# Optimization experiments

Measured on AMD Instinct MI355X. Metric: run time of the kernel, lower is better.

Reference implementation:

```python
import jax, jax.numpy as jnp
import numpy as np

N_NODES = 20000
N_EDGES = 640000
F = 64       # n_features
B = 20       # n_basis
LN_EPS = 1e-5

act = jax.nn.silu

def _lin_init(key, fan_in, fan_out):
    return jax.random.normal(key, (fan_in, fan_out), dtype=jnp.float32) / np.sqrt(fan_in)

def setup_inputs() -> dict:
    key = jax.random.key(0)
    ks = jax.random.split(key, 18)
    inp = {
        "atom_node": jax.random.normal(ks[0], (N_NODES, F), dtype=jnp.float32),
        "force_node": jax.random.normal(ks[1], (N_NODES, 3, F), dtype=jnp.float32),
        "dir_edge": jax.random.normal(ks[2], (N_EDGES, 3), dtype=jnp.float32),
        "dist_edge": jax.random.uniform(ks[3], (N_EDGES, B), dtype=jnp.float32),
        "edge_index": jax.random.randint(ks[4], (2, N_EDGES), 0, N_NODES, dtype=jnp.int64),
        # message_nodepart: Linear(F,F)+act+Linear(F,F)
        "W1": _lin_init(ks[5], F, F), "b1": jnp.zeros((F,), jnp.float32),
        "W2": _lin_init(ks[6], F, F), "b2": jnp.zeros((F,), jnp.float32),
        # message_edgepart: Linear(B,F,bias=False)
        "We": _lin_init(ks[7], B, F),
        # equiv_message1/2: Linear(F,F,nobias)+act+Linear(F,F,nobias)
        "Wq1a": _lin_init(ks[8], F, F), "Wq1b": _lin_init(ks[9], F, F),
        "Wq2a": _lin_init(ks[10], F, F), "Wq2b": _lin_init(ks[11], F, F),
        # equiv_update: Linear(F,F,nobias)
        "Wu": _lin_init(ks[12], F, F),
        # LayerNorm(F)
        "gamma": jnp.ones((F,), jnp.float32), "beta": jnp.zeros((F,), jnp.float32),
    }
    return inp

def reference(atom_node, force_node, dir_edge, dist_edge, edge_index,
              W1, b1, W2, b2, We, Wq1a, Wq1b, Wq2a, Wq2b, Wu, gamma, beta):
    src, dst = edge_index[0], edge_index[1]
    n = atom_node.shape[0]

    # node part of the message: MLP over nodes [N,F]
    mn = act(atom_node @ W1 + b1) @ W2 + b2
    # edge part: [E,F]
    me = dist_edge @ We
    # message: elementwise product of edge part and both endpoint node parts [E,F]
    message = me * mn[src] * mn[dst]

    # invariant update: scatter-add messages to source nodes
    inv_update1 = jax.ops.segment_sum(message, src, num_segments=n)
    atom_node = atom_node + inv_update1

    # equivariant messages [E,3,F]
    em1_inv = act(message @ Wq1a) @ Wq1b            # [E,F]
    em2_inv = act(message @ Wq2a) @ Wq2b            # [E,F]
    equiv_msg = (em1_inv[:, None, :] * dir_edge[:, :, None]
                 + em2_inv[:, None, :] * force_node[dst])  # [E,3,F]
    force_update = jax.ops.segment_sum(equiv_msg, src, num_segments=n)
    force_node = force_node + force_update

    # invariant contraction of vector features: sum over the 3-dim
    inv_update2 = jnp.sum(force_node * (force_node @ Wu), axis=1)  # [N,F]
    atom_node = atom_node + inv_update2

    # LayerNorm over feature dim
    mu = jnp.mean(atom_node, axis=-1, keepdims=True)
    var = jnp.var(atom_node, axis=-1, keepdims=True)
    atom_node = (atom_node - mu) * jax.lax.rsqrt(var + LN_EPS) * gamma + beta

    return (atom_node, force_node)
```

## Files before the change

### kernel.cpp

```cpp
#include <hip/hip_runtime.h>

#define N_NODES 20000
#define N_EDGES 640000
#define FDIM 64
#define NB 20
#define LN_EPS 1e-5f

typedef __attribute__((ext_vector_type(8))) short bf16x8;
typedef __attribute__((ext_vector_type(4))) float f32x4;

#define SEL_HI 0x07060302u
#define SEL_LO 0x05040100u
#define MFMA16 __builtin_amdgcn_mfma_f32_16x16x32_bf16

__device__ __forceinline__ float silu_f(float x) { return x / (1.0f + __expf(-x)); }

__device__ __forceinline__ float bcast_lane(float v, int lane) {
    return __int_as_float(__builtin_amdgcn_readlane(__float_as_int(v), lane));
}

__device__ __forceinline__ unsigned bf16_rn(float x) {
    unsigned u = __float_as_uint(x);
    return (u + 0x7FFFu + ((u >> 16) & 1u)) >> 16;
}

__device__ __forceinline__ unsigned pack_split(float x) {
    unsigned h = bf16_rn(x);
    unsigned lo = bf16_rn(x - __uint_as_float(h << 16));
    return (h << 16) | lo;
}

__device__ __forceinline__ void load_afrag(const unsigned* rowPtr, int kh, int q,
                                           bf16x8* ahi, bf16x8* alo) {
    const uint4 ra = *(const uint4*)(rowPtr + kh * 32 + q * 8);
    const uint4 rb = *(const uint4*)(rowPtr + kh * 32 + q * 8 + 4);
    union { unsigned u[4]; bf16x8 v; } H, L;
    H.u[0] = __builtin_amdgcn_perm(ra.y, ra.x, SEL_HI);
    H.u[1] = __builtin_amdgcn_perm(ra.w, ra.z, SEL_HI);
    H.u[2] = __builtin_amdgcn_perm(rb.y, rb.x, SEL_HI);
    H.u[3] = __builtin_amdgcn_perm(rb.w, rb.z, SEL_HI);
    L.u[0] = __builtin_amdgcn_perm(ra.y, ra.x, SEL_LO);
    L.u[1] = __builtin_amdgcn_perm(ra.w, ra.z, SEL_LO);
    L.u[2] = __builtin_amdgcn_perm(rb.y, rb.x, SEL_LO);
    L.u[3] = __builtin_amdgcn_perm(rb.w, rb.z, SEL_LO);
    *ahi = H.v;
    *alo = L.v;
}

__device__ __forceinline__ void mm3(const unsigned* Bhi, const unsigned* Blo,
                                    bf16x8 ahi, bf16x8 alo, f32x4* acc, int kh, int l) {
#pragma unroll
    for (int c = 0; c < 4; ++c) {
        bf16x8 bh = *(const bf16x8*)(Bhi + (kh * 4 + c) * 256 + l * 4);
        bf16x8 bl = *(const bf16x8*)(Blo + (kh * 4 + c) * 256 + l * 4);
        acc[c] = MFMA16(ahi, bh, acc[c], 0, 0, 0);
        acc[c] = MFMA16(ahi, bl, acc[c], 0, 0, 0);
        acc[c] = MFMA16(alo, bh, acc[c], 0, 0, 0);
    }
}

__global__ __launch_bounds__(256) void node_mlp_kernel(
    const float* __restrict__ atom, const float* __restrict__ W1, const float* __restrict__ b1,
    const float* __restrict__ W2, const float* __restrict__ b2, float* __restrict__ mn)
{
    __shared__ float W1s[FDIM][FDIM];
    __shared__ float W2s[FDIM][FDIM];
    const int f = threadIdx.x, ty = threadIdx.y;
    const int tid = ty * 64 + f;
    for (int i = tid; i < FDIM * FDIM; i += 256) {
        ((float*)W1s)[i] = W1[i];
        ((float*)W2s)[i] = W2[i];
    }
    __syncthreads();
    const float bb1 = b1[f], bb2 = b2[f];
    const int nw = gridDim.x * 4;
    for (int n = blockIdx.x * 4 + ty; n < N_NODES; n += nw) {
        const float a = atom[n * FDIM + f];
        float h = bb1;
        for (int g = 0; g < FDIM; ++g) h += bcast_lane(a, g) * W1s[g][f];
        h = silu_f(h);
        float o = bb2;
        for (int g = 0; g < FDIM; ++g) o += bcast_lane(h, g) * W2s[g][f];
        mn[n * FDIM + f] = o;
    }
}

__global__ __launch_bounds__(1024, 1) void edge_kernel(
    const float* __restrict__ dist,
    const float* __restrict__ dir,
    const int* __restrict__ eidx,
    const float* __restrict__ mn,
    const float* __restrict__ We,
    const float* __restrict__ Wq1a, const float* __restrict__ Wq1b,
    const float* __restrict__ Wq2a, const float* __restrict__ Wq2b,
    const float* __restrict__ forceN,
    float* __restrict__ atomAcc,
    float* __restrict__ forceAcc)
{
    __shared__ __align__(16) unsigned Bfr[16384];
    __shared__ __align__(16) unsigned WeFr[2048];
    __shared__ __align__(16) unsigned Astg[16][16][76];

    const int l = threadIdx.x;
    const int ty = threadIdx.y;
    const int q = l >> 4, row = l & 15;

    for (int t = ty; t < 32; t += 16) {
        const int mm = t >> 3, kh = (t >> 2) & 1, c = t & 3;
        const float* W = (mm == 0) ? Wq1a : (mm == 1) ? Wq2a : (mm == 2) ? Wq1b : Wq2b;
        const int n = c * 16 + row;
        const int kb = kh * 32 + q * 8;
        unsigned* hiP = &Bfr[(((mm * 2 + 0) * 2 + kh) * 4 + c) * 256 + l * 4];
        unsigned* loP = &Bfr[(((mm * 2 + 1) * 2 + kh) * 4 + c) * 256 + l * 4];
#pragma unroll
        for (int i = 0; i < 4; ++i) {
            float w0 = W[(kb + 2 * i) * FDIM + n];
            float w1 = W[(kb + 2 * i + 1) * FDIM + n];
            unsigned h0 = bf16_rn(w0);
            unsigned l0 = bf16_rn(w0 - __uint_as_float(h0 << 16));
            unsigned h1 = bf16_rn(w1);
            unsigned l1 = bf16_rn(w1 - __uint_as_float(h1 << 16));
            hiP[i] = h0 | (h1 << 16);
            loP[i] = l0 | (l1 << 16);
        }
    }
    for (int c = ty; c < 4; c += 16) {
        const int n = c * 16 + row;
        unsigned* hiP = &WeFr[(0 * 4 + c) * 256 + l * 4];
        unsigned* loP = &WeFr[(1 * 4 + c) * 256 + l * 4];
#pragma unroll
        for (int i = 0; i < 4; ++i) {
            const int k0 = q * 8 + 2 * i, k1 = k0 + 1;
            float w0 = (k0 < NB) ? We[k0 * FDIM + n] : 0.0f;
            float w1 = (k1 < NB) ? We[k1 * FDIM + n] : 0.0f;
            unsigned h0 = bf16_rn(w0);
            unsigned l0 = bf16_rn(w0 - __uint_as_float(h0 << 16));
            unsigned h1 = bf16_rn(w1);
            unsigned l1 = bf16_rn(w1 - __uint_as_float(h1 << 16));
            hiP[i] = h0 | (h1 << 16);
            loP[i] = l0 | (l1 << 16);
        }
    }
    __syncthreads();

    const unsigned* B1aH = Bfr + 0 * 2048; const unsigned* B1aL = Bfr + 1 * 2048;
    const unsigned* B2aH = Bfr + 2 * 2048; const unsigned* B2aL = Bfr + 3 * 2048;
    const unsigned* B1bH = Bfr + 4 * 2048; const unsigned* B1bL = Bfr + 5 * 2048;
    const unsigned* B2bH = Bfr + 6 * 2048; const unsigned* B2bL = Bfr + 7 * 2048;
    const unsigned* WeH = WeFr;            const unsigned* WeL = WeFr + 1024;

    unsigned* stg = &Astg[ty][0][0];
    const unsigned* rowPtr = &Astg[ty][row][0];

    const int ngroups = N_EDGES / 16;
    const int stride = gridDim.x * 16;
    int grp = blockIdx.x * 16 + ty;

    int e0 = grp * 16;
    int evA = (l < 32) ? eidx[(l < 16) ? (e0 + l) : (N_EDGES + e0 + (l - 16))] : 0;
    float dvA = (l < 48) ? dir[e0 * 3 + l] : 0.0f;
    float4 daA = {0.f, 0.f, 0.f, 0.f}, dbA = {0.f, 0.f, 0.f, 0.f};
    {
        const float* dp = dist + (size_t)(e0 + row) * NB + q * 8;
        if (q < 2)       { daA = *(const float4*)dp; dbA = *(const float4*)(dp + 4); }
        else if (q == 2) { daA = *(const float4*)dp; }
    }
    float mnS[16], mnD[16];
#pragma unroll
    for (int j = 0; j < 16; ++j) {
        const int src = __builtin_amdgcn_readlane(evA, j);
        const int dst = __builtin_amdgcn_readlane(evA, 16 + j);
        mnS[j] = mn[(size_t)src * FDIM + l];
        mnD[j] = mn[(size_t)dst * FDIM + l];
    }

    while (grp < ngroups) {
        e0 = grp * 16;
        const int grpN = grp + stride;
        const int e0n = (grpN < ngroups) ? grpN * 16 : 0;

        const int evB = (l < 32) ? eidx[(l < 16) ? (e0n + l) : (N_EDGES + e0n + (l - 16))] : 0;
        const float dvB = (l < 48) ? dir[e0n * 3 + l] : 0.0f;

        unsigned s0 = pack_split(daA.x), s1 = pack_split(daA.y);
        unsigned s2 = pack_split(daA.z), s3 = pack_split(daA.w);
        unsigned s4 = pack_split(dbA.x), s5 = pack_split(dbA.y);
        unsigned s6 = pack_split(dbA.z), s7 = pack_split(dbA.w);
        union { unsigned u[4]; bf16x8 v; } AH, AL;
        AH.u[0] = __builtin_amdgcn_perm(s1, s0, SEL_HI);
        AH.u[1] = __builtin_amdgcn_perm(s3, s2, SEL_HI);
        AH.u[2] = __builtin_amdgcn_perm(s5, s4, SEL_HI);
        AH.u[3] = __builtin_amdgcn_perm(s7, s6, SEL_HI);
        AL.u[0] = __builtin_amdgcn_perm(s1, s0, SEL_LO);
        AL.u[1] = __builtin_amdgcn_perm(s3, s2, SEL_LO);
        AL.u[2] = __builtin_amdgcn_perm(s5, s4, SEL_LO);
        AL.u[3] = __builtin_amdgcn_perm(s7, s6, SEL_LO);

        f32x4 me4[4];
#pragma unroll
        for (int c = 0; c < 4; ++c) me4[c] = (f32x4){0.f, 0.f, 0.f, 0.f};
        mm3(WeH, WeL, AH.v, AL.v, me4, 0, l);
#pragma unroll
        for (int c = 0; c < 4; ++c)
#pragma unroll
            for (int r = 0; r < 4; ++r)
                stg[(q * 4 + r) * 76 + (row + 16 * c)] = __float_as_uint(me4[c][r]);

        float4 daB = {0.f, 0.f, 0.f, 0.f}, dbB = {0.f, 0.f, 0.f, 0.f};
        {
            const float* dpn = dist + (size_t)(e0n + row) * NB + q * 8;
            if (q < 2)       { daB = *(const float4*)dpn; dbB = *(const float4*)(dpn + 4); }
            else if (q == 2) { daB = *(const float4*)dpn; }
        }

#pragma unroll
        for (int j = 0; j < 16; ++j) {
            const int src = __builtin_amdgcn_readlane(evA, j);
            const float me = __uint_as_float(stg[j * 76 + l]);
            const float m = me * mnS[j] * mnD[j];
            atomicAdd(&atomAcc[(size_t)src * FDIM + l], m);
            stg[j * 76 + l] = pack_split(m);
        }

#pragma unroll
        for (int j = 0; j < 16; ++j) {
            const int srcN = __builtin_amdgcn_readlane(evB, j);
            const int dstN = __builtin_amdgcn_readlane(evB, 16 + j);
            mnS[j] = mn[(size_t)srcN * FDIM + l];
            mnD[j] = mn[(size_t)dstN * FDIM + l];
        }

        f32x4 acc1[4], acc2[4];
#pragma unroll
        for (int c = 0; c < 4; ++c) {
            acc1[c] = (f32x4){0.f, 0.f, 0.f, 0.f};
            acc2[c] = (f32x4){0.f, 0.f, 0.f, 0.f};
        }
#pragma unroll
        for (int kh = 0; kh < 2; ++kh) {
            bf16x8 ahi, alo;
            load_afrag(rowPtr, kh, q, &ahi, &alo);
            mm3(B1aH, B1aL, ahi, alo, acc1, kh, l);
            mm3(B2aH, B2aL, ahi, alo, acc2, kh, l);
        }
#pragma unroll
        for (int c = 0; c < 4; ++c)
#pragma unroll
            for (int r = 0; r < 4; ++r) {
                acc1[c][r] = silu_f(acc1[c][r]);
                acc2[c][r] = silu_f(acc2[c][r]);
            }

#pragma unroll
        for (int c = 0; c < 4; ++c)
#pragma unroll
            for (int r = 0; r < 4; ++r)
                stg[(q * 4 + r) * 76 + (row + 16 * c)] = pack_split(acc1[c][r]);
        f32x4 eacc1[4];
#pragma unroll
        for (int c = 0; c < 4; ++c) eacc1[c] = (f32x4){0.f, 0.f, 0.f, 0.f};
#pragma unroll
        for (int kh = 0; kh < 2; ++kh) {
            bf16x8 ahi, alo;
            load_afrag(rowPtr, kh, q, &ahi, &alo);
            mm3(B1bH, B1bL, ahi, alo, eacc1, kh, l);
        }

#pragma unroll
        for (int c = 0; c < 4; ++c)
#pragma unroll
            for (int r = 0; r < 4; ++r)
                stg[(q * 4 + r) * 76 + (row + 16 * c)] = pack_split(acc2[c][r]);
        f32x4 eacc2[4];
#pragma unroll
        for (int c = 0; c < 4; ++c) eacc2[c] = (f32x4){0.f, 0.f, 0.f, 0.f};
#pragma unroll
        for (int kh = 0; kh < 2; ++kh) {
            bf16x8 ahi, alo;
            load_afrag(rowPtr, kh, q, &ahi, &alo);
            mm3(B2bH, B2bL, ahi, alo, eacc2, kh, l);
        }

#pragma unroll
        for (int r = 0; r < 4; ++r) {
            const int eo = q * 4 + r;
            const int vs = __shfl(evA, eo);
            const int vd = __shfl(evA, 16 + eo);
            const float d0 = __shfl(dvA, eo * 3 + 0);
            const float d1 = __shfl(dvA, eo * 3 + 1);
            const float d2 = __shfl(dvA, eo * 3 + 2);
            const float* fd = forceN + (size_t)vd * 3 * FDIM;
            float* fa = forceAcc + (size_t)vs * 3 * FDIM;
#pragma unroll
            for (int c = 0; c < 4; ++c) {
                const int n = row + 16 * c;
                const float a = eacc1[c][r];
                const float b = eacc2[c][r];
                atomicAdd(&fa[0 * FDIM + n], a * d0 + b * fd[0 * FDIM + n]);
                atomicAdd(&fa[1 * FDIM + n], a * d1 + b * fd[1 * FDIM + n]);
                atomicAdd(&fa[2 * FDIM + n], a * d2 + b * fd[2 * FDIM + n]);
            }
        }

        evA = evB;
        dvA = dvB;
        daA = daB;
        dbA = dbB;
        grp = grpN;
    }
}

__global__ __launch_bounds__(256) void node_final_kernel(
    const float* __restrict__ Wu, const float* __restrict__ gamma, const float* __restrict__ beta,
    float* __restrict__ atomAcc, const float* __restrict__ forceOut)
{
    __shared__ float Wus[FDIM][FDIM];
    const int f = threadIdx.x, ty = threadIdx.y;
    const int tid = ty * 64 + f;
    for (int i = tid; i < FDIM * FDIM; i += 256) ((float*)Wus)[i] = Wu[i];
    __syncthreads();
    const float gg = gamma[f], bb = beta[f];
    const int nw = gridDim.x * 4;
    for (int n = blockIdx.x * 4 + ty; n < N_NODES; n += nw) {
        const float f0 = forceOut[((size_t)n * 3 + 0) * FDIM + f];
        const float f1 = forceOut[((size_t)n * 3 + 1) * FDIM + f];
        const float f2 = forceOut[((size_t)n * 3 + 2) * FDIM + f];
        float r0 = 0.0f, r1 = 0.0f, r2 = 0.0f;
#pragma unroll 8
        for (int g = 0; g < FDIM; ++g) {
            const float w = Wus[g][f];
            r0 += bcast_lane(f0, g) * w;
            r1 += bcast_lane(f1, g) * w;
            r2 += bcast_lane(f2, g) * w;
        }
        float a = atomAcc[n * FDIM + f] + (f0 * r0 + f1 * r1 + f2 * r2);
        float s = a;
#pragma unroll
        for (int off = 32; off >= 1; off >>= 1) s += __shfl_xor(s, off, 64);
        const float mu = s * (1.0f / 64.0f);
        const float d = a - mu;
        float v = d * d;
#pragma unroll
        for (int off = 32; off >= 1; off >>= 1) v += __shfl_xor(v, off, 64);
        v *= (1.0f / 64.0f);
        atomAcc[n * FDIM + f] = d * rsqrtf(v + LN_EPS) * gg + bb;
    }
}

extern "C" void kernel_launch(void* const* d_in, const int* in_sizes, int n_in,
                              void* d_out, int out_size, void* d_ws, size_t ws_size,
                              hipStream_t stream)
{
    const float* atom_node  = (const float*)d_in[0];
    const float* force_node = (const float*)d_in[1];
    const float* dir_edge   = (const float*)d_in[2];
    const float* dist_edge  = (const float*)d_in[3];
    const int*   edge_index = (const int*)d_in[4];
    const float* W1   = (const float*)d_in[5];
    const float* b1   = (const float*)d_in[6];
    const float* W2   = (const float*)d_in[7];
    const float* b2   = (const float*)d_in[8];
    const float* We   = (const float*)d_in[9];
    const float* Wq1a = (const float*)d_in[10];
    const float* Wq1b = (const float*)d_in[11];
    const float* Wq2a = (const float*)d_in[12];
    const float* Wq2b = (const float*)d_in[13];
    const float* Wu   = (const float*)d_in[14];
    const float* gamma = (const float*)d_in[15];
    const float* beta  = (const float*)d_in[16];

    float* atomOut  = (float*)d_out;
    float* forceOut = (float*)d_out + (size_t)N_NODES * FDIM;
    float* mn = (float*)d_ws;

    hipMemcpyAsync(atomOut, atom_node, (size_t)N_NODES * FDIM * sizeof(float),
                   hipMemcpyDeviceToDevice, stream);
    hipMemcpyAsync(forceOut, force_node, (size_t)N_NODES * 3 * FDIM * sizeof(float),
                   hipMemcpyDeviceToDevice, stream);

    dim3 blk4(64, 4);
    dim3 blk16(64, 16);
    node_mlp_kernel<<<512, blk4, 0, stream>>>(atom_node, W1, b1, W2, b2, mn);
    edge_kernel<<<256, blk16, 0, stream>>>(dist_edge, dir_edge, edge_index, mn, We,
                                           Wq1a, Wq1b, Wq2a, Wq2b, force_node,
                                           atomOut, forceOut);
    node_final_kernel<<<512, blk4, 0, stream>>>(Wu, gamma, beta, atomOut, forceOut);
}
```

Before: 595.5 us.

## Shrink edge blocks to 8 waves, premultiply node parts, batch force gathers before atomics

Edge blocks go from 16 waves to 8, with launch bounds allowing two blocks per CU. The grid stays at 256 blocks, so total concurrent waves drop by half unless occupancy rises. The src and dst node-part values are multiplied at prefetch time, so one register array replaces two, freeing registers. The next dist prefetch moves earlier in the loop, and the force_node gather loads are grouped ahead of the atomic adds to expose more memory parallelism. The risk is less latency hiding from fewer resident waves, since the grid is not enlarged.

```diff
diff --git a/kernel.cpp b/kernel.cpp
--- a/kernel.cpp
+++ b/kernel.cpp
@@ -5,6 +5,7 @@
 #define FDIM 64
 #define NB 20
 #define LN_EPS 1e-5f
+#define NW 8
 
 typedef __attribute__((ext_vector_type(8))) short bf16x8;
 typedef __attribute__((ext_vector_type(4))) float f32x4;
@@ -85,7 +86,7 @@
     }
 }
 
-__global__ __launch_bounds__(1024, 1) void edge_kernel(
+__global__ __launch_bounds__(64 * NW, 2) void edge_kernel(
     const float* __restrict__ dist,
     const float* __restrict__ dir,
     const int* __restrict__ eidx,
@@ -99,13 +100,13 @@
 {
     __shared__ __align__(16) unsigned Bfr[16384];
     __shared__ __align__(16) unsigned WeFr[2048];
-    __shared__ __align__(16) unsigned Astg[16][16][76];
+    __shared__ __align__(16) unsigned Astg[NW][16][76];
 
     const int l = threadIdx.x;
     const int ty = threadIdx.y;
     const int q = l >> 4, row = l & 15;
 
-    for (int t = ty; t < 32; t += 16) {
+    for (int t = ty; t < 32; t += NW) {
         const int mm = t >> 3, kh = (t >> 2) & 1, c = t & 3;
         const float* W = (mm == 0) ? Wq1a : (mm == 1) ? Wq2a : (mm == 2) ? Wq1b : Wq2b;
         const int n = c * 16 + row;
@@ -124,7 +125,7 @@
             loP[i] = l0 | (l1 << 16);
         }
     }
-    for (int c = ty; c < 4; c += 16) {
+    for (int c = ty; c < 4; c += NW) {
         const int n = c * 16 + row;
         unsigned* hiP = &WeFr[(0 * 4 + c) * 256 + l * 4];
         unsigned* loP = &WeFr[(1 * 4 + c) * 256 + l * 4];
@@ -153,8 +154,8 @@
     const unsigned* rowPtr = &Astg[ty][row][0];
 
     const int ngroups = N_EDGES / 16;
-    const int stride = gridDim.x * 16;
-    int grp = blockIdx.x * 16 + ty;
+    const int stride = gridDim.x * NW;
+    int grp = blockIdx.x * NW + ty;
 
     int e0 = grp * 16;
     int evA = (l < 32) ? eidx[(l < 16) ? (e0 + l) : (N_EDGES + e0 + (l - 16))] : 0;
@@ -165,13 +166,12 @@
         if (q < 2)       { daA = *(const float4*)dp; dbA = *(const float4*)(dp + 4); }
         else if (q == 2) { daA = *(const float4*)dp; }
     }
-    float mnS[16], mnD[16];
+    float pA[16];
 #pragma unroll
     for (int j = 0; j < 16; ++j) {
         const int src = __builtin_amdgcn_readlane(evA, j);
         const int dst = __builtin_amdgcn_readlane(evA, 16 + j);
-        mnS[j] = mn[(size_t)src * FDIM + l];
-        mnD[j] = mn[(size_t)dst * FDIM + l];
+        pA[j] = mn[(size_t)src * FDIM + l] * mn[(size_t)dst * FDIM + l];
     }
 
     while (grp < ngroups) {
@@ -181,6 +181,12 @@
 
         const int evB = (l < 32) ? eidx[(l < 16) ? (e0n + l) : (N_EDGES + e0n + (l - 16))] : 0;
         const float dvB = (l < 48) ? dir[e0n * 3 + l] : 0.0f;
+        float4 daB = {0.f, 0.f, 0.f, 0.f}, dbB = {0.f, 0.f, 0.f, 0.f};
+        {
+            const float* dpn = dist + (size_t)(e0n + row) * NB + q * 8;
+            if (q < 2)       { daB = *(const float4*)dpn; dbB = *(const float4*)(dpn + 4); }
+            else if (q == 2) { daB = *(const float4*)dpn; }
+        }
 
         unsigned s0 = pack_split(daA.x), s1 = pack_split(daA.y);
         unsigned s2 = pack_split(daA.z), s3 = pack_split(daA.w);
@@ -206,18 +212,10 @@
             for (int r = 0; r < 4; ++r)
                 stg[(q * 4 + r) * 76 + (row + 16 * c)] = __float_as_uint(me4[c][r]);
 
-        float4 daB = {0.f, 0.f, 0.f, 0.f}, dbB = {0.f, 0.f, 0.f, 0.f};
-        {
-            const float* dpn = dist + (size_t)(e0n + row) * NB + q * 8;
-            if (q < 2)       { daB = *(const float4*)dpn; dbB = *(const float4*)(dpn + 4); }
-            else if (q == 2) { daB = *(const float4*)dpn; }
-        }
-
 #pragma unroll
         for (int j = 0; j < 16; ++j) {
             const int src = __builtin_amdgcn_readlane(evA, j);
-            const float me = __uint_as_float(stg[j * 76 + l]);
-            const float m = me * mnS[j] * mnD[j];
+            const float m = __uint_as_float(stg[j * 76 + l]) * pA[j];
             atomicAdd(&atomAcc[(size_t)src * FDIM + l], m);
             stg[j * 76 + l] = pack_split(m);
         }
@@ -226,8 +224,7 @@
         for (int j = 0; j < 16; ++j) {
             const int srcN = __builtin_amdgcn_readlane(evB, j);
             const int dstN = __builtin_amdgcn_readlane(evB, 16 + j);
-            mnS[j] = mn[(size_t)srcN * FDIM + l];
-            mnD[j] = mn[(size_t)dstN * FDIM + l];
+            pA[j] = mn[(size_t)srcN * FDIM + l] * mn[(size_t)dstN * FDIM + l];
         }
 
         f32x4 acc1[4], acc2[4];
@@ -290,15 +287,21 @@
             const float d1 = __shfl(dvA, eo * 3 + 1);
             const float d2 = __shfl(dvA, eo * 3 + 2);
             const float* fd = forceN + (size_t)vd * 3 * FDIM;
-            float* fa = forceAcc + (size_t)vs * 3 * FDIM;
+            float f0[4], f1[4], f2[4];
 #pragma unroll
             for (int c = 0; c < 4; ++c) {
                 const int n = row + 16 * c;
-                const float a = eacc1[c][r];
-                const float b = eacc2[c][r];
-                atomicAdd(&fa[0 * FDIM + n], a * d0 + b * fd[0 * FDIM + n]);
-                atomicAdd(&fa[1 * FDIM + n], a * d1 + b * fd[1 * FDIM + n]);
-                atomicAdd(&fa[2 * FDIM + n], a * d2 + b * fd[2 * FDIM + n]);
+                f0[c] = fd[0 * FDIM + n];
+                f1[c] = fd[1 * FDIM + n];
+                f2[c] = fd[2 * FDIM + n];
+            }
+            float* fa = forceAcc + (size_t)vs * 3 * FDIM;
+#pragma unroll
+            for (int c = 0; c < 4; ++c) {
+                const int n = row + 16 * c;
+                atomicAdd(&fa[0 * FDIM + n], eacc1[c][r] * d0 + eacc2[c][r] * f0[c]);
+                atomicAdd(&fa[1 * FDIM + n], eacc1[c][r] * d1 + eacc2[c][r] * f1[c]);
+                atomicAdd(&fa[2 * FDIM + n], eacc1[c][r] * d2 + eacc2[c][r] * f2[c]);
             }
         }
 
@@ -379,10 +382,10 @@
                    hipMemcpyDeviceToDevice, stream);
 
     dim3 blk4(64, 4);
-    dim3 blk16(64, 16);
+    dim3 blkE(64, NW);
     node_mlp_kernel<<<512, blk4, 0, stream>>>(atom_node, W1, b1, W2, b2, mn);
-    edge_kernel<<<256, blk16, 0, stream>>>(dist_edge, dir_edge, edge_index, mn, We,
-                                           Wq1a, Wq1b, Wq2a, Wq2b, force_node,
-                                           atomOut, forceOut);
+    edge_kernel<<<256, blkE, 0, stream>>>(dist_edge, dir_edge, edge_index, mn, We,
+                                          Wq1a, Wq1b, Wq2a, Wq2b, force_node,
+                                          atomOut, forceOut);
     node_final_kernel<<<512, blk4, 0, stream>>>(Wu, gamma, beta, atomOut, forceOut);
 }
```

New measurement: 590.1 us. About the same (-0.9%).
